# Kernel optimization log

Hardware: AMD Instinct MI355X
Metric: run time of the kernel (lower is better)

Reference implementation:

```python
import jax, jax.numpy as jnp
import numpy as np

B, S, E = 512, 200, 128
NUM_C = 1024
DIFF = 100


def _glorot(k, shape):
    fan_in, fan_out = shape[-1], shape[0]
    lim = jnp.sqrt(6.0 / (fan_in + fan_out)).astype(jnp.float32)
    return jax.random.uniform(k, shape, jnp.float32, -lim, lim)


def setup_inputs() -> dict:
    key = jax.random.key(0)
    ks = jax.random.split(key, 16)
    c = jax.random.randint(ks[0], (B, S), 0, NUM_C + 1)
    sd = jax.random.randint(ks[1], (B, S), 0, DIFF + 2)
    a = jax.random.randint(ks[2], (B, S), 0, 2)
    cshft = jax.random.randint(ks[3], (B, S), 0, NUM_C + 1)
    sdshft = jax.random.randint(ks[4], (B, S), 0, DIFF + 2)
    # embedding tables (padding_idx=0 rows zeroed, as in nn.Embedding)
    c_table = _glorot(ks[5], (NUM_C + 1, E)).at[0].set(0.0)
    sd_table = _glorot(ks[6], (DIFF + 2, E)).at[0].set(0.0)
    a_table = _glorot(ks[7], (2, E))
    knowledge = _glorot(ks[8], (1, E))  # xavier_uniform [1, E]
    W1 = _glorot(ks[9], (E, 2 * E)); b1 = jnp.zeros((E,), jnp.float32)
    W2 = _glorot(ks[10], (E, E));     b2 = jnp.zeros((E,), jnp.float32)
    W3 = _glorot(ks[11], (E, E));     b3 = jnp.zeros((E,), jnp.float32)
    W4 = _glorot(ks[12], (E, 2 * E)); b4 = jnp.zeros((E,), jnp.float32)
    W5 = _glorot(ks[13], (E, 2 * E)); b5 = jnp.zeros((E,), jnp.float32)
    W6 = _glorot(ks[14], (E, 3 * E)); b6 = jnp.zeros((E,), jnp.float32)
    return dict(c=c, sd=sd, a=a, cshft=cshft, sdshft=sdshft,
                c_table=c_table, sd_table=sd_table, a_table=a_table,
                knowledge=knowledge,
                W1=W1, b1=b1, W2=W2, b2=b2, W3=W3, b3=b3,
                W4=W4, b4=b4, W5=W5, b5=b5, W6=W6, b6=b6)


def reference(c, sd, a, cshft, sdshft, c_table, sd_table, a_table, knowledge,
              W1, b1, W2, b2, W3, b3, W4, b4, W5, b5, W6, b6):
    # embedding lookups: [B, S, E]
    c_emb = c_table[c]
    sd_emb = sd_table[sd]
    a_emb = a_table[a]
    target_c = c_table[cshft]
    target_sd = sd_table[sdshft]

    input_data = jnp.concatenate((c_emb, sd_emb), -1) @ W1.T + b1      # [B,S,E]
    target_data = jnp.concatenate((target_c, target_sd), -1) @ W1.T + b1

    k0 = jnp.broadcast_to(knowledge, (c.shape[0], knowledge.shape[-1]))  # [B,E]

    def step(k, xs):
        sd_t, a_t, in_t = xs                       # each [B,E]
        qq = k - in_t
        gates_SDF = jax.nn.sigmoid(qq @ W2.T + b2)
        SDFt = gates_SDF * jnp.tanh(qq @ W3.T + b3)  # dropout = eval-mode identity
        x = jnp.concatenate((SDFt, a_t), -1)
        gates_PKA = jax.nn.sigmoid(x @ W4.T + b4)
        PKAt = gates_PKA * jnp.tanh(x @ W5.T + b5)
        ins = jnp.concatenate((k, a_t, sd_t), -1)
        gates_KSU = jax.nn.sigmoid(ins @ W6.T + b6)
        k_new = gates_KSU * k + (1.0 - gates_KSU) * PKAt
        return k_new, k_new

    xs = (jnp.swapaxes(sd_emb, 0, 1),      # [S,B,E]
          jnp.swapaxes(a_emb, 0, 1),
          jnp.swapaxes(input_data, 0, 1))
    _, hs = jax.lax.scan(step, k0, xs)     # hs: [S,B,E]
    output = jnp.swapaxes(hs, 0, 1)        # [B,S,E]

    logits = jnp.sum(target_data * output, axis=-1)  # [B,S]
    return jax.nn.sigmoid(logits)
```

## Files before the change

kernel.cpp:

```cpp
#include <hip/hip_runtime.h>


#define S_ 200
#define E_ 128
#define RS 136

typedef float  float4v __attribute__((ext_vector_type(4)));
typedef _Float16 f16x8 __attribute__((ext_vector_type(8)));

#define BAR() asm volatile("s_waitcnt lgkmcnt(0)\n\ts_barrier" ::: "memory")

__device__ __forceinline__ float fast_sigmoid(float x) {
  return __builtin_amdgcn_rcpf(1.f + __expf(-x));
}
__device__ __forceinline__ float fast_tanh(float x) {
  return 2.f * __builtin_amdgcn_rcpf(1.f + __expf(-2.f * x)) - 1.f;
}

#define DPP_ADD(x, ctrl) \
  ((x) + __builtin_bit_cast(float, __builtin_amdgcn_update_dpp( \
       0, __builtin_bit_cast(int, (x)), (ctrl), 0xf, 0xf, true)))

__device__ __forceinline__ f16x8 cvt8(const float* __restrict__ p) {
  float4v a = *(const float4v*)p;
  float4v b = *(const float4v*)(p + 4);
  f16x8 r;
  r[0] = (_Float16)a[0]; r[1] = (_Float16)a[1];
  r[2] = (_Float16)a[2]; r[3] = (_Float16)a[3];
  r[4] = (_Float16)b[0]; r[5] = (_Float16)b[1];
  r[6] = (_Float16)b[2]; r[7] = (_Float16)b[3];
  return r;
}

__global__ __launch_bounds__(256) void dimkt_prep(
    const float* __restrict__ c_table, const float* __restrict__ sd_table,
    const float* __restrict__ a_table,
    const float* __restrict__ W1, const float* __restrict__ b1,
    const float* __restrict__ W4, const float* __restrict__ b4,
    const float* __restrict__ W5, const float* __restrict__ b5,
    const float* __restrict__ W6, const float* __restrict__ b6,
    float* __restrict__ ws) {
  __shared__ __attribute__((aligned(16))) float s_src[8][E_];
  __shared__ float s_w[E_][33];
  const int blk = blockIdx.x, t = threadIdx.x;
  const int e = t & 127, h = t >> 7;
  const float* src; const float* wb; const float* bias; float* dst;
  int r0, maxrow, wstr, woff;
  if (blk < 129)      { r0 = blk * 8;       src = c_table;  maxrow = 1024; wb = W1; wstr = 256; woff = 0;   bias = nullptr; dst = ws; }
  else if (blk < 142) { r0 = (blk-129) * 8; src = sd_table; maxrow = 101;  wb = W1; wstr = 256; woff = 128; bias = b1;      dst = ws + 131200; }
  else if (blk < 155) { r0 = (blk-142) * 8; src = sd_table; maxrow = 101;  wb = W6; wstr = 384; woff = 256; bias = nullptr; dst = ws + 144256; }
  else if (blk == 155){ r0 = 0;             src = a_table;  maxrow = 1;    wb = W4; wstr = 256; woff = 128; bias = b4;      dst = ws + 157312; }
  else if (blk == 156){ r0 = 0;             src = a_table;  maxrow = 1;    wb = W5; wstr = 256; woff = 128; bias = b5;      dst = ws + 157568; }
  else                { r0 = 0;             src = a_table;  maxrow = 1;    wb = W6; wstr = 384; woff = 128; bias = b6;      dst = ws + 157824; }
  #pragma unroll
  for (int i = 0; i < 4; ++i) {
    int idx = i * 256 + t, row = idx >> 7, col = idx & 127;
    int rr = r0 + row; if (rr > maxrow) rr = maxrow;
    s_src[row][col] = src[rr * E_ + col];
  }
  float binit = bias ? bias[e] : 0.f;
  float acc[4] = {binit, binit, binit, binit};
  for (int k0 = 0; k0 < 4; ++k0) {
    __syncthreads();
    #pragma unroll
    for (int i = 0; i < 16; ++i) {
      int idx = i * 256 + t;
      s_w[idx >> 5][idx & 31] = wb[(idx >> 5) * wstr + woff + k0 * 32 + (idx & 31)];
    }
    __syncthreads();
    #pragma unroll 4
    for (int kk = 0; kk < 32; ++kk) {
      float wv = s_w[e][kk];
      #pragma unroll
      for (int g = 0; g < 4; ++g)
        acc[g] += wv * s_src[h * 4 + g][k0 * 32 + kk];
    }
  }
  #pragma unroll
  for (int g = 0; g < 4; ++g) {
    int row = r0 + h * 4 + g;
    if (row <= maxrow) dst[row * E_ + e] = acc[g];
  }
}

__global__ __launch_bounds__(512, 2) void dimkt_scan(
    const int* __restrict__ c, const int* __restrict__ sd, const int* __restrict__ a,
    const int* __restrict__ cshft, const int* __restrict__ sdshft,
    const float* __restrict__ knowledge,
    const float* __restrict__ W2, const float* __restrict__ b2,
    const float* __restrict__ W3, const float* __restrict__ b3,
    const float* __restrict__ W4, const float* __restrict__ W5,
    const float* __restrict__ W6,
    const float* __restrict__ ws, float* __restrict__ out) {

  const float* __restrict__ C1  = ws;
  const float* __restrict__ SD1 = ws + 131200;
  const float* __restrict__ SD6 = ws + 144256;
  const float* __restrict__ A4  = ws + 157312;
  const float* __restrict__ A5  = ws + 157568;
  const float* __restrict__ A6  = ws + 157824;

  const int tid  = threadIdx.x;
  const int w    = tid >> 6;
  const int lane = tid & 63;
  const int l15  = lane & 15;
  const int q    = lane >> 4;
  const int qodd = q & 1;
  const int e    = w * 16 + l15;
  const int j    = q >> 1;
  const int bj   = blockIdx.x * 2 + j;

  __shared__ __attribute__((aligned(16))) _Float16 A1[16 * RS];
  __shared__ __attribute__((aligned(16))) _Float16 A2[16 * RS];
  __shared__ __attribute__((aligned(32))) int idx_lds[S_][2][8];
  __shared__ float part[8][2][S_];

  for (int i = tid; i < 2 * S_; i += 512) {
    const int jj = (i >= S_) ? 1 : 0;
    const int ss = jj ? (i - S_) : i;
    const int src = (blockIdx.x * 2 + jj) * S_ + ss;
    idx_lds[ss][jj][0] = c[src];
    idx_lds[ss][jj][1] = sd[src];
    idx_lds[ss][jj][2] = a[src];
    idx_lds[ss][jj][3] = cshft[src];
    idx_lds[ss][jj][4] = sdshft[src];
  }

  const int stq = (j * 8) * RS + e;
  const int stk = stq + RS;
  const int rd0 = l15 * RS + q * 8;
  const bool m1 = (l15 & 6) == 0;
  const bool m2 = (l15 & 7) == 0;

  f16x8 w2f[4], w3f[4], w4f[4], w5f[4], w6f[4];
  #pragma unroll
  for (int t = 0; t < 4; ++t) {
    const int ko = t * 32 + q * 8;
    w2f[t] = cvt8(W2 + e * 128 + ko);
    w3f[t] = cvt8(W3 + e * 128 + ko);
    w4f[t] = cvt8(W4 + e * 256 + ko);
    w5f[t] = cvt8(W5 + e * 256 + ko);
    w6f[t] = cvt8(W6 + e * 384 + ko);
  }
  const float b2e = b2[e], b3e = b3[e];
  const float A4t0 = A4[e], A4t1 = A4[E_ + e];
  const float A5t0 = A5[e], A5t1 = A5[E_ + e];
  const float A6t0 = A6[e], A6t1 = A6[E_ + e];

  float kreg = knowledge[e];

  const int base = bj * S_;
  int ic = c[base], isd = sd[base], ia = a[base], ict = cshft[base], ist = sdshft[base];
  float inT  = C1[ic * E_ + e] + SD1[isd * E_ + e];
  float sd6v = SD6[isd * E_ + e];
  float a4v = ia ? A4t1 : A4t0;
  float a5v = ia ? A5t1 : A5t0;
  float a6v = ia ? A6t1 : A6t0;
  float tgt  = C1[ict * E_ + e] + SD1[ist * E_ + e];
  int nic = c[base + 1], nisd = sd[base + 1], nia = a[base + 1],
      nict = cshft[base + 1], nist = sdshft[base + 1];

  __syncthreads();
  if (!qodd) {
    A1[stq] = (_Float16)(kreg - inT);
    A1[stk] = (_Float16)kreg;
  }
  __syncthreads();

  f16x8 f0{}, f1{}, f2{}, f3{};
  f16x8 g0{}, g1{}, g2v{}, g3{};

  float4v acc2{0.f,0.f,0.f,0.f}, acc3{0.f,0.f,0.f,0.f}, acc6{0.f,0.f,0.f,0.f};
  float4v acc4{0.f,0.f,0.f,0.f}, acc5{0.f,0.f,0.f,0.f};

  float pprev = 0.f;
  int   sprev = 0;

  #pragma unroll 1
  for (int s = 0; s < S_; ++s) {
    if (m1) {
      f0 = *(const f16x8*)&A1[rd0];
      f1 = *(const f16x8*)&A1[rd0 + 32];
      f2 = *(const f16x8*)&A1[rd0 + 64];
      f3 = *(const f16x8*)&A1[rd0 + 96];
    }

    if (s > 0) {
      float pr = pprev;
      pr = DPP_ADD(pr, 0x111);
      pr = DPP_ADD(pr, 0x112);
      pr = DPP_ADD(pr, 0x114);
      pr = DPP_ADD(pr, 0x118);
      if (l15 == 15 && !qodd) part[w][j][sprev] = pr;
    }

    float ninT = C1[nic * E_ + e] + SD1[nisd * E_ + e];
    float nsd6 = SD6[nisd * E_ + e];
    float na4 = nia ? A4t1 : A4t0;
    float na5 = nia ? A5t1 : A5t0;
    float na6 = nia ? A6t1 : A6t0;
    float ntg  = C1[nict * E_ + e] + SD1[nist * E_ + e];

    const int s2 = (s + 2 < S_) ? (s + 2) : (S_ - 1);
    const int4 iv = *(const int4*)&idx_lds[s2][j][0];
    const int tist = idx_lds[s2][j][4];

    acc2[0] = b2e;
    acc3[0] = b3e;
    acc2 = __builtin_amdgcn_mfma_f32_16x16x32_f16(f0, w2f[0], acc2, 0, 0, 0);
    acc3 = __builtin_amdgcn_mfma_f32_16x16x32_f16(f0, w3f[0], acc3, 0, 0, 0);
    acc2 = __builtin_amdgcn_mfma_f32_16x16x32_f16(f1, w2f[1], acc2, 0, 0, 0);
    acc3 = __builtin_amdgcn_mfma_f32_16x16x32_f16(f1, w3f[1], acc3, 0, 0, 0);
    acc2 = __builtin_amdgcn_mfma_f32_16x16x32_f16(f2, w2f[2], acc2, 0, 0, 0);
    acc3 = __builtin_amdgcn_mfma_f32_16x16x32_f16(f2, w3f[2], acc3, 0, 0, 0);
    acc2 = __builtin_amdgcn_mfma_f32_16x16x32_f16(f3, w2f[3], acc2, 0, 0, 0);
    acc3 = __builtin_amdgcn_mfma_f32_16x16x32_f16(f3, w3f[3], acc3, 0, 0, 0);

    acc6[1] = a6v + sd6v;
    acc6 = __builtin_amdgcn_mfma_f32_16x16x32_f16(f0, w6f[0], acc6, 0, 0, 0);
    acc6 = __builtin_amdgcn_mfma_f32_16x16x32_f16(f1, w6f[1], acc6, 0, 0, 0);

    const float g2  = fast_sigmoid(acc2[0]);
    const float th3 = fast_tanh(acc3[0]);
    const float sdfv = g2 * th3;
    if (!qodd) A2[stq] = (_Float16)sdfv;

    acc6 = __builtin_amdgcn_mfma_f32_16x16x32_f16(f2, w6f[2], acc6, 0, 0, 0);
    acc6 = __builtin_amdgcn_mfma_f32_16x16x32_f16(f3, w6f[3], acc6, 0, 0, 0);

    BAR();

    if (m2) {
      g0  = *(const f16x8*)&A2[rd0];
      g1  = *(const f16x8*)&A2[rd0 + 32];
      g2v = *(const f16x8*)&A2[rd0 + 64];
      g3  = *(const f16x8*)&A2[rd0 + 96];
    }

    const float g6 = fast_sigmoid(acc6[1]);

    acc4[0] = a4v;
    acc4 = __builtin_amdgcn_mfma_f32_16x16x32_f16(g0, w4f[0], acc4, 0, 0, 0);
    acc4 = __builtin_amdgcn_mfma_f32_16x16x32_f16(g1, w4f[1], acc4, 0, 0, 0);
    acc4 = __builtin_amdgcn_mfma_f32_16x16x32_f16(g2v, w4f[2], acc4, 0, 0, 0);
    acc4 = __builtin_amdgcn_mfma_f32_16x16x32_f16(g3, w4f[3], acc4, 0, 0, 0);
    acc5[0] = a5v;
    acc5 = __builtin_amdgcn_mfma_f32_16x16x32_f16(g0, w5f[0], acc5, 0, 0, 0);
    acc5 = __builtin_amdgcn_mfma_f32_16x16x32_f16(g1, w5f[1], acc5, 0, 0, 0);

    const float s4 = fast_sigmoid(acc4[0]);

    acc5 = __builtin_amdgcn_mfma_f32_16x16x32_f16(g2v, w5f[2], acc5, 0, 0, 0);
    acc5 = __builtin_amdgcn_mfma_f32_16x16x32_f16(g3, w5f[3], acc5, 0, 0, 0);

    const float t5  = fast_tanh(acc5[0]);
    const float pka = s4 * t5;
    const float knew = pka + g6 * (kreg - pka);
    kreg = knew;
    if (!qodd) {
      A1[stq] = (_Float16)(knew - ninT);
      A1[stk] = (_Float16)knew;
    }

    pprev = tgt * knew;
    sprev = s;

    inT = ninT; sd6v = nsd6; a4v = na4; a5v = na5; a6v = na6; tgt = ntg;
    nic = iv.x; nisd = iv.y; nia = iv.z; nict = iv.w; nist = tist;

    BAR();
  }

  {
    float pr = pprev;
    pr = DPP_ADD(pr, 0x111);
    pr = DPP_ADD(pr, 0x112);
    pr = DPP_ADD(pr, 0x114);
    pr = DPP_ADD(pr, 0x118);
    if (l15 == 15 && !qodd) part[w][j][sprev] = pr;
  }

  __syncthreads();
  for (int i = tid; i < 2 * S_; i += 512) {
    const int jj = (i >= S_) ? 1 : 0;
    const int ss = jj ? (i - S_) : i;
    float logit = 0.f;
    #pragma unroll
    for (int x = 0; x < 8; ++x) logit += part[x][jj][ss];
    out[(blockIdx.x * 2 + jj) * S_ + ss] = fast_sigmoid(logit);
  }
}

extern "C" void kernel_launch(void* const* d_in, const int* in_sizes, int n_in,
                              void* d_out, int out_size, void* d_ws, size_t ws_size,
                              hipStream_t stream) {
  const int*   c         = (const int*)  d_in[0];
  const int*   sd        = (const int*)  d_in[1];
  const int*   a         = (const int*)  d_in[2];
  const int*   cshft     = (const int*)  d_in[3];
  const int*   sdshft    = (const int*)  d_in[4];
  const float* c_table   = (const float*)d_in[5];
  const float* sd_table  = (const float*)d_in[6];
  const float* a_table   = (const float*)d_in[7];
  const float* knowledge = (const float*)d_in[8];
  const float* W1 = (const float*)d_in[9];  const float* b1 = (const float*)d_in[10];
  const float* W2 = (const float*)d_in[11]; const float* b2 = (const float*)d_in[12];
  const float* W3 = (const float*)d_in[13]; const float* b3 = (const float*)d_in[14];
  const float* W4 = (const float*)d_in[15]; const float* b4 = (const float*)d_in[16];
  const float* W5 = (const float*)d_in[17]; const float* b5 = (const float*)d_in[18];
  const float* W6 = (const float*)d_in[19]; const float* b6 = (const float*)d_in[20];
  float* ws  = (float*)d_ws;
  float* out = (float*)d_out;
  (void)in_sizes; (void)n_in; (void)out_size; (void)ws_size;

  dimkt_prep<<<158, 256, 0, stream>>>(c_table, sd_table, a_table,
                                      W1, b1, W4, b4, W5, b5, W6, b6, ws);
  dimkt_scan<<<256, 512, 0, stream>>>(c, sd, a, cshft, sdshft, knowledge,
                                      W2, b2, W3, b3, W4, W5, W6, ws, out);
}
```

Measured before the change: 260.4 us.

## Split next-step gathers across paired lanes and shorten the gate dependency chain

Even and odd lanes now each gather one of the two embedding sums (input or target) instead of both. The partner's value is exchanged with a ds_swizzle lane-xor, which halves the per-step global loads in the recurrent loop. The tanh calls are folded algebraically into the sigmoid products, and g6*k and 1-g6 are precomputed so the final k update is a single FMA on the critical path. The loop is also unrolled by two. This relies on the odd/even lane pairing matching the xor-1 swizzle, and the unroll adds register pressure.

```diff
diff --git a/kernel.cpp b/kernel.cpp
--- a/kernel.cpp
+++ b/kernel.cpp
@@ -12,9 +12,6 @@
 
 __device__ __forceinline__ float fast_sigmoid(float x) {
   return __builtin_amdgcn_rcpf(1.f + __expf(-x));
-}
-__device__ __forceinline__ float fast_tanh(float x) {
-  return 2.f * __builtin_amdgcn_rcpf(1.f + __expf(-2.f * x)) - 1.f;
 }
 
 #define DPP_ADD(x, ctrl) \
@@ -176,7 +173,7 @@
   float pprev = 0.f;
   int   sprev = 0;
 
-  #pragma unroll 1
+  #pragma unroll 2
   for (int s = 0; s < S_; ++s) {
     if (m1) {
       f0 = *(const f16x8*)&A1[rd0];
@@ -194,12 +191,14 @@
       if (l15 == 15 && !qodd) part[w][j][sprev] = pr;
     }
 
-    float ninT = C1[nic * E_ + e] + SD1[nisd * E_ + e];
-    float nsd6 = SD6[nisd * E_ + e];
-    float na4 = nia ? A4t1 : A4t0;
-    float na5 = nia ? A5t1 : A5t0;
-    float na6 = nia ? A6t1 : A6t0;
-    float ntg  = C1[nict * E_ + e] + SD1[nist * E_ + e];
+    const int selc  = qodd ? nict : nic;
+    const int selsd = qodd ? nist : nisd;
+    const float L1 = C1[selc * E_ + e];
+    const float L2 = SD1[selsd * E_ + e];
+    const float nsd6 = SD6[nisd * E_ + e];
+    const float na4 = nia ? A4t1 : A4t0;
+    const float na5 = nia ? A5t1 : A5t0;
+    const float na6 = nia ? A6t1 : A6t0;
 
     const int s2 = (s + 2 < S_) ? (s + 2) : (S_ - 1);
     const int4 iv = *(const int4*)&idx_lds[s2][j][0];
@@ -221,8 +220,9 @@
     acc6 = __builtin_amdgcn_mfma_f32_16x16x32_f16(f1, w6f[1], acc6, 0, 0, 0);
 
     const float g2  = fast_sigmoid(acc2[0]);
-    const float th3 = fast_tanh(acc3[0]);
-    const float sdfv = g2 * th3;
+    const float G2  = g2 + g2;
+    const float sg3 = __builtin_amdgcn_rcpf(1.f + __expf(-2.f * acc3[0]));
+    const float sdfv = G2 * sg3 - g2;
     if (!qodd) A2[stq] = (_Float16)sdfv;
 
     acc6 = __builtin_amdgcn_mfma_f32_16x16x32_f16(f2, w6f[2], acc6, 0, 0, 0);
@@ -238,6 +238,8 @@
     }
 
     const float g6 = fast_sigmoid(acc6[1]);
+    const float gk = g6 * kreg;
+    const float h6 = 1.f - g6;
 
     acc4[0] = a4v;
     acc4 = __builtin_amdgcn_mfma_f32_16x16x32_f16(g0, w4f[0], acc4, 0, 0, 0);
@@ -248,24 +250,30 @@
     acc5 = __builtin_amdgcn_mfma_f32_16x16x32_f16(g0, w5f[0], acc5, 0, 0, 0);
     acc5 = __builtin_amdgcn_mfma_f32_16x16x32_f16(g1, w5f[1], acc5, 0, 0, 0);
 
-    const float s4 = fast_sigmoid(acc4[0]);
+    const float s4  = fast_sigmoid(acc4[0]);
+    const float S42 = s4 + s4;
 
     acc5 = __builtin_amdgcn_mfma_f32_16x16x32_f16(g2v, w5f[2], acc5, 0, 0, 0);
     acc5 = __builtin_amdgcn_mfma_f32_16x16x32_f16(g3, w5f[3], acc5, 0, 0, 0);
 
-    const float t5  = fast_tanh(acc5[0]);
-    const float pka = s4 * t5;
-    const float knew = pka + g6 * (kreg - pka);
+    const float sg5 = __builtin_amdgcn_rcpf(1.f + __expf(-2.f * acc5[0]));
+    const float pka = S42 * sg5 - s4;
+    const float knew = pka * h6 + gk;
     kreg = knew;
+
+    const float sum = L1 + L2;
+    const float ntg = __builtin_bit_cast(float,
+        __builtin_amdgcn_ds_swizzle(__builtin_bit_cast(int, sum), 0x401F));
+
     if (!qodd) {
-      A1[stq] = (_Float16)(knew - ninT);
+      A1[stq] = (_Float16)(knew - sum);
       A1[stk] = (_Float16)knew;
     }
 
     pprev = tgt * knew;
     sprev = s;
 
-    inT = ninT; sd6v = nsd6; a4v = na4; a5v = na5; a6v = na6; tgt = ntg;
+    sd6v = nsd6; a4v = na4; a5v = na5; a6v = na6; tgt = ntg;
     nic = iv.x; nisd = iv.y; nia = iv.z; nict = iv.w; nist = tist;
 
     BAR();
```

Result: faster. 252.9 us (-2.9%).
